# Kernel tuning notes

Hardware: AMD Instinct MI355X
Metric: run time of the kernel (lower is better)

The kernel has to match this reference:

```python
import jax, jax.numpy as jnp
import numpy as np


def setup_inputs() -> dict:
    key = jax.random.key(0)
    k1, k2, k3, k4 = jax.random.split(key, 4)
    B, S, K, R, DIN, DOUT = 8, 2048, 16, 16, 2048, 2048
    h = jax.random.normal(k1, (B, S, DIN), dtype=jnp.float32)
    alpha = jax.random.uniform(k2, (B, K), dtype=jnp.float32)
    A_bank = jax.random.normal(k3, (K, R, DIN), dtype=jnp.float32) * (1.0 / np.sqrt(DIN))
    B_bank = jax.random.normal(k4, (K, DOUT, R), dtype=jnp.float32) * (1.0 / np.sqrt(R))
    return {"h": h, "alpha": alpha, "A_bank": A_bank, "B_bank": B_bank}


def reference(h, alpha, A_bank, B_bank):
    # Mix K low-rank bases per sample, then apply low-rank delta to h.
    A_mixed = jnp.einsum('bk,kri->bri', alpha, A_bank)   # [B, r, d_in]
    B_mixed = jnp.einsum('bk,kor->bor', alpha, B_bank)   # [B, d_out, r]
    z = jnp.einsum('bri,bsi->bsr', A_mixed, h)           # [B, S, r]
    delta = jnp.einsum('bor,bsr->bso', B_mixed, z)       # [B, S, d_out]
    return delta
```

## Files before the change

### kernel.cpp

```cpp
#include <hip/hip_runtime.h>

typedef unsigned int u32;
typedef float f32x4 __attribute__((ext_vector_type(4)));

#define BB 8
#define SS 2048
#define KK 16
#define RR 16
#define DIN 2048
#define DOUT 2048

__global__ void __launch_bounds__(256) mix_kernel(
    const float* __restrict__ alpha,
    const float* __restrict__ A_bank,
    const float* __restrict__ B_bank,
    float* __restrict__ Am,
    float* __restrict__ Bm)
{
    int t = blockIdx.x * 256 + threadIdx.x;
    const int half = BB * RR * DIN;
    if (t < half) {
        int i = t & (DIN - 1);
        int r = (t >> 11) & (RR - 1);
        int b = t >> 15;
        float acc = 0.f;
#pragma unroll
        for (int k = 0; k < KK; ++k)
            acc += alpha[b * KK + k] * A_bank[(k * RR + r) * DIN + i];
        Am[t] = acc;
    } else {
        int u = t - half;
        int r = u & (RR - 1);
        int o = (u >> 4) & (DOUT - 1);
        int b = u >> 15;
        float acc = 0.f;
#pragma unroll
        for (int k = 0; k < KK; ++k)
            acc += alpha[b * KK + k] * B_bank[(k * DOUT + o) * RR + r];
        Bm[u] = acc;
    }
}

__global__ void __launch_bounds__(256, 3) fused_kernel(
    const float* __restrict__ h,
    const float* __restrict__ Am,
    const float* __restrict__ Bm,
    float* __restrict__ out)
{
    __shared__ float zt[8 * 16];

    int b = blockIdx.y;
    int wid = threadIdx.x >> 6;
    int lane = threadIdx.x & 63;
    int s0 = blockIdx.x * 8;
    int sw = s0 + wid * 2;

    const float* hb = h + (size_t)b * SS * DIN + (size_t)sw * DIN;
    const float* Ab = Am + (size_t)b * RR * DIN;

    float a[32];
#pragma unroll
    for (int v = 0; v < 32; ++v) a[v] = 0.f;

#pragma unroll 1
    for (int t = 0; t < 8; ++t) {
        int i0 = t * 256 + lane * 4;
        f32x4 hv0 = __builtin_nontemporal_load((const f32x4*)(hb + i0));
        f32x4 hv1 = __builtin_nontemporal_load((const f32x4*)(hb + DIN + i0));
#pragma unroll
        for (int r = 0; r < 16; ++r) {
            f32x4 av = *(const f32x4*)(Ab + r * DIN + i0);
            a[r]      += hv0.x * av.x + hv0.y * av.y + hv0.z * av.z + hv0.w * av.w;
            a[16 + r] += hv1.x * av.x + hv1.y * av.y + hv1.z * av.z + hv1.w * av.w;
        }
    }

#pragma unroll
    for (int off = 16; off >= 1; off >>= 1) {
        bool up = (lane & off) != 0;
#pragma unroll
        for (int v = 0; v < off; ++v) {
            float send = up ? a[v] : a[v + off];
            float keep = up ? a[v + off] : a[v];
            a[v] = keep + __shfl_xor(send, off, 64);
        }
    }
    a[0] += __shfl_xor(a[0], 32, 64);
    if (lane < 32) zt[wid * 32 + lane] = a[0];
    __syncthreads();

    float* op = out + ((size_t)b * SS + s0) * DOUT;

#pragma unroll 1
    for (int oc = 0; oc < 2; ++oc) {
        int o0 = oc * 1024 + threadIdx.x * 4;
        const float* wp = Bm + ((size_t)b * DOUT + o0) * RR;
        float w[4][16];
#pragma unroll
        for (int j = 0; j < 4; ++j) {
#pragma unroll
            for (int q = 0; q < 4; ++q) {
                f32x4 p = *(const f32x4*)(wp + j * RR + q * 4);
                w[j][q * 4 + 0] = p.x; w[j][q * 4 + 1] = p.y;
                w[j][q * 4 + 2] = p.z; w[j][q * 4 + 3] = p.w;
            }
        }
#pragma unroll 4
        for (int s = 0; s < 8; ++s) {
            float zz[16];
#pragma unroll
            for (int q = 0; q < 4; ++q) {
                f32x4 zv = *(const f32x4*)(zt + s * 16 + q * 4);
                zz[q * 4 + 0] = zv.x; zz[q * 4 + 1] = zv.y;
                zz[q * 4 + 2] = zv.z; zz[q * 4 + 3] = zv.w;
            }
            float rj[4];
#pragma unroll
            for (int j = 0; j < 4; ++j) {
                float acc = 0.f;
#pragma unroll
                for (int r = 0; r < 16; ++r) acc += w[j][r] * zz[r];
                rj[j] = acc;
            }
            f32x4 res;
            res.x = rj[0]; res.y = rj[1]; res.z = rj[2]; res.w = rj[3];
            __builtin_nontemporal_store(res, (f32x4*)(op + (size_t)s * DOUT + o0));
        }
    }
}

extern "C" void kernel_launch(void* const* d_in, const int* in_sizes, int n_in,
                              void* d_out, int out_size, void* d_ws, size_t ws_size,
                              hipStream_t stream)
{
    const float* h      = (const float*)d_in[0];
    const float* alpha  = (const float*)d_in[1];
    const float* A_bank = (const float*)d_in[2];
    const float* B_bank = (const float*)d_in[3];
    float* out = (float*)d_out;

    float* Am = (float*)d_ws;
    float* Bm = Am + BB * RR * DIN;

    mix_kernel<<<2048, 256, 0, stream>>>(alpha, A_bank, B_bank, Am, Bm);
    fused_kernel<<<dim3(256, 8), 256, 0, stream>>>(h, Am, Bm, out);
}
```

Measured before the change: 288.0 us.

## Register-tile h·A projection 4x4 per lane with software-pipelined loads, 128-thread blocks

The fused kernel now uses 128 threads (2 waves), each wave handling 4 sequence rows. Each lane computes a 4-row by 4-rank register tile over a 16-lane slice of d_in. Loads of h and Am are double-buffered in registers so the next chunk's loads are issued before the current chunk's FMAs. This raises arithmetic intensity per loaded Am/h value and shortens the shuffle reduction, at the cost of more live registers and fewer threads per block for the output phase, which now takes four output chunks.

```diff
diff --git a/kernel.cpp b/kernel.cpp
--- a/kernel.cpp
+++ b/kernel.cpp
@@ -41,7 +41,7 @@
     }
 }
 
-__global__ void __launch_bounds__(256, 3) fused_kernel(
+__global__ void __launch_bounds__(128, 4) fused_kernel(
     const float* __restrict__ h,
     const float* __restrict__ Am,
     const float* __restrict__ Bm,
@@ -50,34 +50,62 @@
     __shared__ float zt[8 * 16];
 
     int b = blockIdx.y;
-    int wid = threadIdx.x >> 6;
-    int lane = threadIdx.x & 63;
+    int tid = threadIdx.x;
+    int wid = tid >> 6;
+    int lane = tid & 63;
+    int il = lane & 15;
+    int rg = lane >> 4;
     int s0 = blockIdx.x * 8;
-    int sw = s0 + wid * 2;
+    int sw = s0 + wid * 4;
 
-    const float* hb = h + (size_t)b * SS * DIN + (size_t)sw * DIN;
-    const float* Ab = Am + (size_t)b * RR * DIN;
+    const float* hl = h + ((size_t)b * SS + sw) * DIN + il * 4;
+    const float* al = Am + ((size_t)b * RR + rg * 4) * DIN + il * 4;
 
-    float a[32];
+    float a[16];
 #pragma unroll
-    for (int v = 0; v < 32; ++v) a[v] = 0.f;
+    for (int v = 0; v < 16; ++v) a[v] = 0.f;
+
+    f32x4 h0[4], h1[4], av0[4], av1[4];
+#pragma unroll
+    for (int j = 0; j < 4; ++j)
+        h0[j] = __builtin_nontemporal_load((const f32x4*)(hl + (size_t)j * DIN));
+#pragma unroll
+    for (int q = 0; q < 4; ++q)
+        av0[q] = *(const f32x4*)(al + (size_t)q * DIN);
 
 #pragma unroll 1
-    for (int t = 0; t < 8; ++t) {
-        int i0 = t * 256 + lane * 4;
-        f32x4 hv0 = __builtin_nontemporal_load((const f32x4*)(hb + i0));
-        f32x4 hv1 = __builtin_nontemporal_load((const f32x4*)(hb + DIN + i0));
+    for (int c = 0; c < 32; c += 2) {
 #pragma unroll
-        for (int r = 0; r < 16; ++r) {
-            f32x4 av = *(const f32x4*)(Ab + r * DIN + i0);
-            a[r]      += hv0.x * av.x + hv0.y * av.y + hv0.z * av.z + hv0.w * av.w;
-            a[16 + r] += hv1.x * av.x + hv1.y * av.y + hv1.z * av.z + hv1.w * av.w;
+        for (int j = 0; j < 4; ++j)
+            h1[j] = __builtin_nontemporal_load((const f32x4*)(hl + (size_t)j * DIN + (c + 1) * 64));
+#pragma unroll
+        for (int q = 0; q < 4; ++q)
+            av1[q] = *(const f32x4*)(al + (size_t)q * DIN + (c + 1) * 64);
+#pragma unroll
+        for (int q = 0; q < 4; ++q)
+#pragma unroll
+            for (int j = 0; j < 4; ++j)
+                a[j * 4 + q] += h0[j].x * av0[q].x + h0[j].y * av0[q].y +
+                                h0[j].z * av0[q].z + h0[j].w * av0[q].w;
+        if (c + 2 < 32) {
+#pragma unroll
+            for (int j = 0; j < 4; ++j)
+                h0[j] = __builtin_nontemporal_load((const f32x4*)(hl + (size_t)j * DIN + (c + 2) * 64));
+#pragma unroll
+            for (int q = 0; q < 4; ++q)
+                av0[q] = *(const f32x4*)(al + (size_t)q * DIN + (c + 2) * 64);
         }
+#pragma unroll
+        for (int q = 0; q < 4; ++q)
+#pragma unroll
+            for (int j = 0; j < 4; ++j)
+                a[j * 4 + q] += h1[j].x * av1[q].x + h1[j].y * av1[q].y +
+                                h1[j].z * av1[q].z + h1[j].w * av1[q].w;
     }
 
 #pragma unroll
-    for (int off = 16; off >= 1; off >>= 1) {
-        bool up = (lane & off) != 0;
+    for (int off = 8; off >= 1; off >>= 1) {
+        bool up = (il & off) != 0;
 #pragma unroll
         for (int v = 0; v < off; ++v) {
             float send = up ? a[v] : a[v + off];
@@ -85,15 +113,14 @@
             a[v] = keep + __shfl_xor(send, off, 64);
         }
     }
-    a[0] += __shfl_xor(a[0], 32, 64);
-    if (lane < 32) zt[wid * 32 + lane] = a[0];
+    zt[(wid * 4 + (il >> 2)) * 16 + rg * 4 + (il & 3)] = a[0];
     __syncthreads();
 
     float* op = out + ((size_t)b * SS + s0) * DOUT;
 
 #pragma unroll 1
-    for (int oc = 0; oc < 2; ++oc) {
-        int o0 = oc * 1024 + threadIdx.x * 4;
+    for (int oc = 0; oc < 4; ++oc) {
+        int o0 = oc * 512 + tid * 4;
         const float* wp = Bm + ((size_t)b * DOUT + o0) * RR;
         float w[4][16];
 #pragma unroll
@@ -143,5 +170,5 @@
     float* Bm = Am + BB * RR * DIN;
 
     mix_kernel<<<2048, 256, 0, stream>>>(alpha, A_bank, B_bank, Am, Bm);
-    fused_kernel<<<dim3(256, 8), 256, 0, stream>>>(h, Am, Bm, out);
+    fused_kernel<<<dim3(256, 8), 128, 0, stream>>>(h, Am, Bm, out);
 }
```

Result: no change. 283.1 us (-1.7%).
